# Kernel optimization log

Hardware: AMD Instinct MI355X
Metric: run time of the kernel (lower is better)

## Reference

```python
import jax, jax.numpy as jnp
import numpy as np

B, T, F_, S, H = 4096, 128, 96, 128, 512
IMPUTE_WEIGHT = 0.3
L1, L2 = 0.01, 0.1


def setup_inputs() -> dict:
    key = jax.random.key(0)
    ks = jax.random.split(key, 28)
    def n(k, shape, s=0.05):
        return jax.random.normal(k, shape, jnp.float32) * s
    return dict(
        values=jax.random.normal(ks[0], (B, T, F_), jnp.float32),
        masks=jax.random.bernoulli(ks[1], 0.8, (B, T, F_)).astype(jnp.float32),
        deltas=jax.random.uniform(ks[2], (B, T, F_), jnp.float32, 0.0, 5.0),
        statics=jax.random.normal(ks[3], (B, S), jnp.float32),
        static_masks=jax.random.bernoulli(ks[4], 0.8, (B, S)).astype(jnp.float32),
        labels=jax.random.bernoulli(ks[5], 0.5, (B,)).astype(jnp.float32),
        fr_W=n(ks[6], (S, S)), fr_b=n(ks[7], (S,)),
        d1_W=n(ks[8], (H, S)), d1_b=n(ks[9], (H,)),
        d2_W=n(ks[10], (H, H)), d2_b=n(ks[11], (H,)),
        d3_W=n(ks[12], (H, H)), d3_b=n(ks[13], (H,)),
        td_W=n(ks[14], (H, F_)), td_b=n(ks[15], (H,)),
        hist_W=n(ks[16], (F_, H)), hist_b=n(ks[17], (F_,)),
        st_W=n(ks[18], (F_, S)), st_b=n(ks[19], (F_,)),
        real_W=n(ks[20], (F_, F_)), real_b=n(ks[21], (F_,)),
        lstm_Wih=n(ks[22], (4 * H, 2 * F_)), lstm_Whh=n(ks[23], (4 * H, H)),
        lstm_bih=n(ks[24], (4 * H,)), lstm_bhh=n(ks[25], (4 * H,)),
        out_W=n(ks[26], (1, H)), out_b=n(ks[27], (1,)),
    )


def reference(values, masks, deltas, statics, static_masks, labels,
              fr_W, fr_b, d1_W, d1_b, d2_W, d2_b, d3_W, d3_b,
              td_W, td_b, hist_W, hist_b, st_W, st_b, real_W, real_b,
              lstm_Wih, lstm_Whh, lstm_bih, lstm_bhh, out_W, out_b):
    sg = jax.lax.stop_gradient
    # ---- MultiModal (dropout = identity in inference) ----
    s_h = statics @ fr_W.T + fr_b
    s_c = static_masks * statics + (1.0 - static_masks) * s_h
    s_tc = s_c
    s_loss = jnp.sum(jnp.abs(statics - s_c) * static_masks) / (jnp.sum(static_masks) + 1e-5)
    s_loss = s_loss + IMPUTE_WEIGHT * L2 * jnp.sum(jnp.abs(jnp.diagonal(sg(fr_W))))
    h = jax.nn.relu(s_c @ d1_W.T + d1_b)
    h = jax.nn.relu(h @ d2_W.T + d2_b)
    h = jax.nn.relu(h @ d3_W.T + d3_b)                 # initial hidden state
    c = jnp.zeros((values.shape[0], H), values.dtype)
    st_term = s_tc @ st_W.T + st_b

    def step(carry, xs):
        h, c, xl = carry
        x, m, d = xs                                   # each [B, F_]
        gamma = jnp.exp(-jax.nn.relu(d @ td_W.T + td_b))
        h = h * gamma
        x_c = (x @ real_W.T + real_b) + (h @ hist_W.T + hist_b) + st_term
        xl = xl + jnp.sum(jnp.abs(x - x_c) * m) / (jnp.sum(m) + 1e-5)
        c_c = m * x + (1.0 - m) * x_c
        inp = jnp.concatenate([c_c, m], axis=1)        # [B, 2*F_]
        gates = inp @ lstm_Wih.T + lstm_bih + h @ lstm_Whh.T + lstm_bhh
        i, f, g, o = jnp.split(gates, 4, axis=1)       # torch LSTMCell gate order
        c = jax.nn.sigmoid(f) * c + jax.nn.sigmoid(i) * jnp.tanh(g)
        h = jax.nn.sigmoid(o) * jnp.tanh(c)
        return (h, c, xl), c_c

    xs = (jnp.swapaxes(values, 0, 1), jnp.swapaxes(masks, 0, 1), jnp.swapaxes(deltas, 0, 1))
    (h, c, x_loss), imps = jax.lax.scan(step, (h, c, jnp.float32(0.0)), xs)
    imputations = jnp.swapaxes(imps, 0, 1)             # [B, T, F_]

    y_h = h @ out_W.T + out_b                          # [B, 1]
    z = y_h[:, 0]
    # BCE with logits, mean reduction (stable form)
    y_loss = jnp.mean(jnp.maximum(z, 0.0) - z * labels + jnp.log1p(jnp.exp(-jnp.abs(z))))
    # regularizers on .data (stop-gradient in torch semantics)
    r_loss = L1 * (jnp.sum(jnp.abs(sg(real_W))) + jnp.sum(jnp.abs(sg(hist_W))) + jnp.sum(jnp.abs(sg(st_W))))
    r_loss = r_loss + L2 * jnp.sum(jnp.abs(jnp.diagonal(sg(real_W))))
    loss = y_loss + r_loss + IMPUTE_WEIGHT * x_loss + s_loss
    return (loss, jax.nn.sigmoid(y_h), imputations)
```

## Files before the change

### kernel.cpp

```cpp
#include <hip/hip_runtime.h>
#include <math.h>

#define Bn 4096
#define Tn 128
#define Fn 96
#define Sn 128
#define Hn 512

typedef __attribute__((ext_vector_type(8))) short bf16x8;
typedef __attribute__((ext_vector_type(4))) float f32x4;

#define GC(p) ((const __attribute__((address_space(1))) void*)(p))
#define LC(p) ((__attribute__((address_space(3))) void*)(p))

__device__ __forceinline__ short tobf(float f){
  unsigned u = __float_as_uint(f);
  unsigned r = (u + 0x7fffu + ((u>>16)&1u)) >> 16;
  return (short)r;
}
__device__ __forceinline__ float bf2f(short s){
  return __uint_as_float(((unsigned)(unsigned short)s)<<16);
}
__device__ __forceinline__ float sigmf_(float x){ return 1.0f/(1.0f+expf(-x)); }

__device__ __forceinline__ int haddr(int row, int k){
  int c = k & 63;
  return ((k>>6)<<10) + (row<<6) + ((((c>>3) ^ (row&7)))<<3) + (c&7);
}
__device__ __forceinline__ int haddr128(int row, int k){
  int c = k & 63;
  return ((k>>6)<<13) + (row<<6) + ((((c>>3) ^ (row&7)))<<3) + (c&7);
}

__device__ __forceinline__ void stage_tile(const short* gsrc, size_t sstride, int k0,
                                           short* lt, int rows, int wid, int lane, int nw){
  int calls = rows >> 3;
  for (int c = wid; c < calls; c += nw){
    int r = (c<<3) + (lane>>3);
    int ch = (lane&7) ^ (r&7);
    const short* gp = gsrc + (size_t)r*sstride + k0 + (ch<<3);
    __builtin_amdgcn_global_load_lds(GC(gp), LC(lt + (c<<9)), 16, 0, 0);
  }
}
__device__ __forceinline__ bf16x8 frag(const short* lt, int row, int ch){
  return *(const bf16x8*)(lt + (row<<6) + ((ch ^ (row&7))<<3));
}


__global__ void k_pack_td(const float* __restrict__ tdW, short* __restrict__ tdWp){
  int i = blockIdx.x*256 + threadIdx.x;
  if (i >= 512*128) return;
  int n = i>>7, k = i&127;
  tdWp[i] = (k < Fn) ? tobf(tdW[n*Fn + k]) : (short)0;
}
__global__ void k_pack_x(const float* __restrict__ realW, const float* __restrict__ histW,
                         const float* __restrict__ realb, const float* __restrict__ histb,
                         short* __restrict__ Wxp, float* __restrict__ bxp){
  int i = blockIdx.x*256 + threadIdx.x;
  if (i < Fn) bxp[i] = realb[i] + histb[i];
  if (i >= Fn*640) return;
  int f = i/640, k = i - f*640;
  float v = 0.f;
  if (k < 512) v = histW[f*Hn + k];
  else if (k < 608) v = realW[f*Fn + (k-512)];
  Wxp[i] = tobf(v);
}
__global__ void k_pack_g(const float* __restrict__ Wih, const float* __restrict__ Whh,
                         const float* __restrict__ bih, const float* __restrict__ bhh,
                         short* __restrict__ Wgp, float* __restrict__ bgp){
  int i = blockIdx.x*256 + threadIdx.x;
  if (i >= 16*128*704) return;
  int k = i % 704; int nc = i / 704;
  int pb = nc >> 7, ncol = nc & 127;
  int jj = pb*32 + (ncol >> 2), g = ncol & 3;
  int n = g*Hn + jj;
  float v;
  if (k < 512) v = Whh[(size_t)n*Hn + k];
  else if (k < 608) v = Wih[(size_t)n*192 + (k-512)];
  else v = Wih[(size_t)n*192 + 96 + (k-608)];
  Wgp[i] = tobf(v);
  if (k == 0) bgp[nc] = bih[n] + bhh[n];
}
__global__ void k_cvt(const float* __restrict__ src, short* __restrict__ dst, int n){
  int i = blockIdx.x*256 + threadIdx.x;
  if (i < n) dst[i] = tobf(src[i]);
}


__global__ void k_static(const float* __restrict__ statics, const float* __restrict__ smask,
                         const float* __restrict__ frW, const float* __restrict__ frb,
                         float* __restrict__ s_c){
  __shared__ float row[Sn];
  int b = blockIdx.x, j = threadIdx.x;
  row[j] = statics[b*Sn + j];
  __syncthreads();
  float acc = frb[j];
  #pragma unroll 4
  for (int k = 0; k < Sn; k++) acc += row[k] * frW[j*Sn + k];
  float m = smask[b*Sn + j];
  s_c[b*Sn + j] = m * row[j] + (1.0f - m) * acc;
}

template<int K, bool RELU, bool WF32>
__global__ __launch_bounds__(512) void k_gemm(const short* __restrict__ A,
    const short* __restrict__ B, const float* __restrict__ bias,
    short* __restrict__ outb, float* __restrict__ outf){
  __shared__ __align__(16) short stA[2][8192], stB[2][8192];
  const int tid = threadIdx.x, lane = tid&63, wid = tid>>6;
  const int mb = blockIdx.x >> 2, nb = blockIdx.x & 3;
  const int r0 = mb*128, c0 = nb*128;
  const int wM = wid>>1, wN = wid&1, lr = lane&15, lq = lane>>4;
  f32x4 acc[2][4];
  #pragma unroll
  for (int m=0;m<2;m++)
    #pragma unroll
    for (int n=0;n<4;n++) acc[m][n] = (f32x4){0,0,0,0};
  constexpr int NS = K/64;
  stage_tile(A + (size_t)r0*K, K, 0, stA[0], 128, wid, lane, 8);
  stage_tile(B + (size_t)c0*K, K, 0, stB[0], 128, wid, lane, 8);
  __syncthreads();
  for (int kc=0; kc<NS; kc++){
    if (kc < NS-1){
      stage_tile(A + (size_t)r0*K, K, (kc+1)*64, stA[(kc+1)&1], 128, wid, lane, 8);
      stage_tile(B + (size_t)c0*K, K, (kc+1)*64, stB[(kc+1)&1], 128, wid, lane, 8);
    }
    #pragma unroll
    for (int kk=0;kk<2;kk++){
      int ch = (kk<<2) + lq;
      bf16x8 af[2];
      #pragma unroll
      for (int m=0;m<2;m++) af[m] = frag(stA[kc&1], wM*32 + m*16 + lr, ch);
      #pragma unroll
      for (int n=0;n<4;n++){
        bf16x8 bf = frag(stB[kc&1], wN*64 + n*16 + lr, ch);
        #pragma unroll
        for (int m=0;m<2;m++)
          acc[m][n] = __builtin_amdgcn_mfma_f32_16x16x32_bf16(af[m], bf, acc[m][n],0,0,0);
      }
    }
    __syncthreads();
  }
  #pragma unroll
  for (int m=0;m<2;m++)
    #pragma unroll
    for (int n=0;n<4;n++){
      int col = c0 + wN*64 + n*16 + lr;
      float bv = bias[col];
      #pragma unroll
      for (int reg=0;reg<4;reg++){
        int row = r0 + wM*32 + m*16 + (lq<<2) + reg;
        float v = acc[m][n][reg] + bv;
        if (RELU) v = fmaxf(v, 0.f);
        outb[(size_t)row*512 + col] = tobf(v);
        if (WF32) outf[(size_t)row*512 + col] = v;
      }
    }
}

template<int K, int N, bool RELU>
__global__ void k_mlp(const float* __restrict__ in, const float* __restrict__ W,
                      const float* __restrict__ bias, float* __restrict__ out){
  __shared__ float row[K];
  int b = blockIdx.x;
  for (int i = threadIdx.x; i < K; i += blockDim.x) row[i] = in[b*K + i];
  __syncthreads();
  for (int n = threadIdx.x; n < N; n += blockDim.x){
    float acc = bias[n];
    #pragma unroll 4
    for (int k = 0; k < K; k++) acc += row[k] * W[n*K + k];
    if (RELU) acc = fmaxf(acc, 0.0f);
    out[b*N + n] = acc;
  }
}

__global__ __launch_bounds__(512) void k_dec0(
    const float* __restrict__ deltas, const short* __restrict__ tdWp,
    const float* __restrict__ tdb, const float* __restrict__ h_g,
    short* __restrict__ inp){
  __shared__ __align__(16) short Adel[2*1024];
  __shared__ __align__(16) short Bbig[65536];
  const int tid = threadIdx.x, lane = tid&63, wid = tid>>6;
  const int r0 = blockIdx.x*16;
  const int lr = lane&15, lq = lane>>4;

  float4 dv4;
  const bool act = tid < 384;
  int ar=0, af0=0;
  if (act){
    ar = tid/24; af0 = (tid - ar*24)*4;
    dv4 = *(const float4*)(deltas + (size_t)(r0+ar)*Tn*Fn + af0);
  }
  float hreg[16];
  #pragma unroll
  for (int nq=0;nq<4;nq++){
    int col = nq*128 + wid*16 + lr;
    #pragma unroll
    for (int reg=0;reg<4;reg++)
      hreg[nq*4+reg] = h_g[(size_t)(r0 + (lq<<2) + reg)*Hn + col];
  }
  #pragma unroll
  for (int s=0; s<8; s++)
    stage_tile(tdWp + (size_t)((s>>1)*128)*128, 128, (s&1)*64, Bbig + s*8192, 128, wid, lane, 8);
  if (act){
    #pragma unroll
    for (int j=0;j<4;j++)
      Adel[haddr(ar, af0+j)] = tobf(((const float*)&dv4)[j]);
  }
  { int r = tid>>5, cz = tid&31; Adel[haddr(r, 96+cz)] = 0; }
  __syncthreads();

  f32x4 accd[4];
  #pragma unroll
  for (int q=0;q<4;q++) accd[q] = (f32x4){0,0,0,0};
  #pragma unroll
  for (int s=0; s<8; s++){
    int nq = s>>1, kc = s&1;
    #pragma unroll
    for (int kk=0;kk<2;kk++){
      int ch = (kk<<2) + lq;
      bf16x8 afr = frag(Adel + kc*1024, lr, ch);
      bf16x8 bfr = frag(Bbig + s*8192, wid*16 + lr, ch);
      accd[nq] = __builtin_amdgcn_mfma_f32_16x16x32_bf16(afr, bfr, accd[nq], 0,0,0);
    }
  }
  #pragma unroll
  for (int nq=0;nq<4;nq++){
    int col = nq*128 + wid*16 + lr;
    float tb = tdb[col];
    #pragma unroll
    for (int reg=0;reg<4;reg++){
      int row = (lq<<2) + reg;
      float v = accd[nq][reg] + tb;
      inp[(size_t)(r0+row)*704 + col] = tobf(hreg[nq*4+reg] * __expf(-fmaxf(v,0.f)));
    }
  }
}

__global__ __launch_bounds__(512) void k_xc2(int t,
    const float* __restrict__ values, const float* __restrict__ masks,
    const short* __restrict__ Wxp,  const float* __restrict__ bxp,
    const float* __restrict__ st,
    short* __restrict__ inp, float* __restrict__ out_imp,
    float* __restrict__ num, float* __restrict__ den){
  __shared__ __align__(16) short A2[10*1024];
  __shared__ short sm[16*96];
  __shared__ __align__(16) short Bbig[61440];
  __shared__ float wred[8], wred2[8];
  const int tid = threadIdx.x, lane = tid&63, wid = tid>>6;
  const int r0 = blockIdx.x*16;
  const int lr = lane&15, lq = lane>>4;

  float4 xv4, mv4;
  const bool act = tid < 384;
  int ar=0, af0=0;
  if (act){
    ar = tid/24; af0 = (tid - ar*24)*4;
    size_t gb = ((size_t)(r0+ar)*Tn + t)*Fn + af0;
    xv4 = *(const float4*)(values + gb);
    mv4 = *(const float4*)(masks  + gb);
  }
  float streg[4] = {0.f,0.f,0.f,0.f};
  if (wid < 6){
    int f = wid*16 + lr;
    #pragma unroll
    for (int reg=0;reg<4;reg++)
      streg[reg] = st[(size_t)(r0 + (lq<<2) + reg)*Fn + f];
  }

  for (int c2 = wid; c2 < 16; c2 += 8){
    int chunk = c2 >> 1, rg = c2 & 1;
    int r = rg*8 + (lane>>3);
    int ch = (lane&7) ^ (r&7);
    const short* gp = inp + (size_t)(r0 + r)*704 + chunk*64 + (ch<<3);
    __builtin_amdgcn_global_load_lds(GC(gp), LC(A2 + chunk*1024 + rg*512), 16, 0, 0);
  }
  #pragma unroll
  for (int kx=0; kx<10; kx++)
    stage_tile(Wxp, 640, kx*64, Bbig + kx*6144, 96, wid, lane, 8);

  if (act){
    #pragma unroll
    for (int j=0;j<4;j++){
      int f = af0 + j;
      float xv = ((const float*)&xv4)[j];
      float mv = ((const float*)&mv4)[j];
      sm[ar*96 + f] = tobf(mv);
      inp[(size_t)(r0+ar)*704 + 608 + f] = tobf(mv);
      A2[haddr(ar, 512+f)] = tobf(xv);
    }
  }
  { int r = tid>>5, cz = tid&31; A2[haddr(r, 608+cz)] = 0; }
  __syncthreads();

  f32x4 accx = (f32x4){0,0,0,0};
  if (wid < 6){
    #pragma unroll
    for (int kx=0; kx<10; kx++)
      #pragma unroll
      for (int kk=0;kk<2;kk++){
        int ch = (kk<<2) + lq;
        bf16x8 afr = frag(A2 + kx*1024, lr, ch);
        bf16x8 bfr = frag(Bbig + kx*6144, wid*16 + lr, ch);
        accx = __builtin_amdgcn_mfma_f32_16x16x32_bf16(afr, bfr, accx, 0,0,0);
      }
  }
  float lsum = 0.f, msum = 0.f;
  if (wid < 6){
    int f = wid*16 + lr;
    float bx = bxp[f];
    #pragma unroll
    for (int reg=0;reg<4;reg++){
      int row = (lq<<2) + reg;
      float xcv = accx[reg] + bx + streg[reg];
      float xv = bf2f(A2[haddr(row, 512+f)]);
      float mv = bf2f(sm[row*96 + f]);
      lsum += fabsf(xv - xcv)*mv;
      msum += mv;
      float cc = mv*xv + (1.f-mv)*xcv;
      inp[(size_t)(r0+row)*704 + 512 + f] = tobf(cc);
      out_imp[((size_t)(r0+row)*Tn + t)*Fn + f] = cc;
    }
  }
  #pragma unroll
  for (int o=32;o>0;o>>=1){ lsum += __shfl_down(lsum, o); msum += __shfl_down(msum, o); }
  if (lane==0){ wred[wid] = lsum; wred2[wid] = msum; }
  __syncthreads();
  if (tid==0){
    float s2 = 0.f, s3 = 0.f;
    #pragma unroll
    for (int w2=0;w2<8;w2++){ s2 += wred[w2]; s3 += wred2[w2]; }
    atomicAdd(&num[t], s2);
    atomicAdd(&den[t], s3);
  }
}

__global__ __launch_bounds__(512, 4) void k_gates(int t,
    const short* __restrict__ inpR, short* __restrict__ inpW,
    const short* __restrict__ Wgp, const float* __restrict__ bgp,
    const float* __restrict__ deltas, const short* __restrict__ tdWp,
    const float* __restrict__ tdb,
    float* __restrict__ h_g, float* __restrict__ c_g){
  __shared__ __align__(16) short SMEM[32768];
  const int tid = threadIdx.x, lane = tid&63, wid = tid>>6;
  const int mb = blockIdx.x & 31, pb = blockIdx.x >> 5;
  const int r0 = mb*128;
  const short* gA = inpR + (size_t)r0*704;
  const short* gB = Wgp + (size_t)pb*128*704;
  const int wM = wid>>1, wN = wid&1, lr = lane&15, lq = lane>>4;
  const bool hg = (t+1 < Tn);
  f32x4 acc[2][4];
  #pragma unroll
  for (int m=0;m<2;m++)
    #pragma unroll
    for (int n=0;n<4;n++) acc[m][n] = (f32x4){0,0,0,0};

  stage_tile(gA, 704, 0, SMEM, 128, wid, lane, 8);
  stage_tile(gB, 704, 0, SMEM + 16384, 128, wid, lane, 8);
  __syncthreads();

  for (int kc=0; kc<11; kc++){
    if (kc < 10){
      stage_tile(gA, 704, (kc+1)*64, SMEM + ((kc+1)&1)*8192, 128, wid, lane, 8);
      stage_tile(gB, 704, (kc+1)*64, SMEM + 16384 + ((kc+1)&1)*8192, 128, wid, lane, 8);
    }
    #pragma unroll
    for (int kk=0;kk<2;kk++){
      int ch = (kk<<2) + lq;
      bf16x8 af[2];
      #pragma unroll
      for (int m=0;m<2;m++) af[m] = frag(SMEM + (kc&1)*8192, wM*32 + m*16 + lr, ch);
      #pragma unroll
      for (int n=0;n<4;n++){
        bf16x8 bf = frag(SMEM + 16384 + (kc&1)*8192, wN*64 + n*16 + lr, ch);
        #pragma unroll
        for (int m=0;m<2;m++)
          acc[m][n] = __builtin_amdgcn_mfma_f32_16x16x32_bf16(af[m], bf, acc[m][n],0,0,0);
      }
    }
    __syncthreads();
  }

  float dreg[24];
  const int drow = tid>>2, dc0 = (tid&3)*24;
  if (hg){
    size_t gb = ((size_t)(r0+drow)*Tn + (t+1))*Fn + dc0;
    #pragma unroll
    for (int q=0;q<6;q++){
      float4 v4 = *(const float4*)(deltas + gb + q*4);
      dreg[q*4+0]=v4.x; dreg[q*4+1]=v4.y; dreg[q*4+2]=v4.z; dreg[q*4+3]=v4.w;
    }
    stage_tile(tdWp + (size_t)(pb*32)*128, 128, 0,  SMEM + 16384, 32, wid, lane, 8);
    stage_tile(tdWp + (size_t)(pb*32)*128, 128, 64, SMEM + 18432, 32, wid, lane, 8);
  }

  const int g = lane&3;
  const float s_  = (g==2) ? 2.0f : -1.0f;
  const float ca_ = (g==2) ? -2.0f : 1.0f;
  const float cb_ = (g==2) ? 1.0f : 0.0f;
  float hnew[2][4];
  #pragma unroll
  for (int m=0;m<2;m++){
    int row = r0 + wM*32 + m*16 + (lq<<2) + g;
    #pragma unroll
    for (int n=0;n<4;n++){
      int colbase = wN*64 + n*16 + lr;
      float b = bgp[pb*128 + colbase];
      float q0 = 1.f/(1.f+__expf(s_*(acc[m][n][0]+b))); float a0 = q0*ca_+cb_;
      float q1 = 1.f/(1.f+__expf(s_*(acc[m][n][1]+b))); float a1 = q1*ca_+cb_;
      float q2 = 1.f/(1.f+__expf(s_*(acc[m][n][2]+b))); float a2 = q2*ca_+cb_;
      float q3 = 1.f/(1.f+__expf(s_*(acc[m][n][3]+b))); float a3 = q3*ca_+cb_;
      int i1=g^1, i2=g^2, i3=g^3;
      float p1 = (i1==0)?a0:(i1==1)?a1:(i1==2)?a2:a3;
      float p2 = (i2==0)?a0:(i2==1)?a1:(i2==2)?a2:a3;
      float p3 = (i3==0)?a0:(i3==1)?a1:(i3==2)?a2:a3;
      float ow = (g==0)?a0:(g==1)?a1:(g==2)?a2:a3;
      float t1 = __shfl_xor(p1, 1, 64);
      float t2 = __shfl_xor(p2, 2, 64);
      float t3 = __shfl_xor(p3, 3, 64);
      float si = (g==0)?ow:(g==1)?t1:(g==2)?t2:t3;
      float sf = (g==1)?ow:(g==0)?t1:(g==3)?t2:t3;
      float tg = (g==2)?ow:(g==3)?t1:(g==0)?t2:t3;
      float so = (g==3)?ow:(g==2)?t1:(g==1)?t2:t3;
      int jh = pb*32 + (colbase>>2);
      size_t idx = (size_t)row*Hn + jh;
      float co = c_g[idx];
      float cn = sf*co + si*tg;
      float targ = fminf(fmaxf(2.0f*cn,-60.f),60.f);
      float e = __expf(targ); float th = (e-1.f)/(e+1.f);
      c_g[idx] = cn;
      float hv = so*th;
      h_g[idx] = hv;
      hnew[m][n] = hv;
    }
  }

  if (hg){
    #pragma unroll
    for (int j=0;j<24;j++){
      int cdx = dc0 + j;
      SMEM[haddr128(drow, cdx)] = tobf(dreg[j]);
    }
    #pragma unroll
    for (int j=0;j<8;j++){
      int cdx = 96 + (tid&3)*8 + j;
      SMEM[haddr128(drow, cdx)] = 0;
    }
    __syncthreads();

    f32x4 gv[2];
    gv[0]=(f32x4){0,0,0,0}; gv[1]=(f32x4){0,0,0,0};
    #pragma unroll
    for (int kc=0;kc<2;kc++)
      #pragma unroll
      for (int kk=0;kk<2;kk++){
        int ch = (kk<<2) + lq;
        bf16x8 afr = frag(SMEM + kc*8192, wid*16 + lr, ch);
        #pragma unroll
        for (int n=0;n<2;n++)
          gv[n] = __builtin_amdgcn_mfma_f32_16x16x32_bf16(afr,
                    frag(SMEM + 16384 + kc*2048, n*16 + lr, ch), gv[n], 0,0,0);
      }
    float* vlds = (float*)(SMEM + 20480);
    #pragma unroll
    for (int n=0;n<2;n++)
      #pragma unroll
      for (int reg=0;reg<4;reg++)
        vlds[(wid*16 + (lq<<2) + reg)*33 + n*16 + lr] = gv[n][reg];
    __syncthreads();

    #pragma unroll
    for (int m=0;m<2;m++){
      int rowl = wM*32 + m*16 + (lq<<2) + g;
      #pragma unroll
      for (int n=0;n<4;n++){
        int jl = (wN*64 + n*16 + lr)>>2;
        float v = vlds[rowl*33 + jl] + tdb[pb*32 + jl];
        float gam = __expf(-fmaxf(v, 0.f));
        inpW[(size_t)(r0+rowl)*704 + pb*32 + jl] = tobf(hnew[m][n] * gam);
      }
    }
  }
}


__global__ void k_out(const float* __restrict__ h_g, const float* __restrict__ outW,
                      const float* __restrict__ outb, const float* __restrict__ labels,
                      float* __restrict__ out_sig, float* __restrict__ yacc){
  int b = blockIdx.x, lane = threadIdx.x;
  float s = 0.f;
  for (int k = lane; k < Hn; k += 64) s += h_g[(size_t)b*Hn + k] * outW[k];
  #pragma unroll
  for (int o = 32; o > 0; o >>= 1) s += __shfl_down(s, o);
  if (lane == 0){
    float z = s + outb[0];
    out_sig[b] = sigmf_(z);
    float yl = fmaxf(z, 0.f) - z*labels[b] + log1pf(expf(-fabsf(z)));
    atomicAdd(yacc, yl);
  }
}

__global__ void k_loss(const float* __restrict__ realW, const float* __restrict__ histW,
                       const float* __restrict__ stW,   const float* __restrict__ frW,
                       const float* __restrict__ num,   const float* __restrict__ den,
                       const float* __restrict__ yacc,  float* __restrict__ out0){
  int tid = threadIdx.x;
  float r1 = 0.f;
  for (int i = tid; i < Fn*Fn; i += 256) r1 += fabsf(realW[i]);
  for (int i = tid; i < Fn*Hn; i += 256) r1 += fabsf(histW[i]);
  for (int i = tid; i < Fn*Sn; i += 256) r1 += fabsf(stW[i]);
  float rd = 0.f;
  for (int i = tid; i < Fn; i += 256) rd += fabsf(realW[i*Fn + i]);
  float fd = 0.f;
  for (int i = tid; i < Sn; i += 256) fd += fabsf(frW[i*Sn + i]);
  float xl = 0.f;
  for (int t = tid; t < Tn; t += 256) xl += num[t] / (den[t] + 1e-5f);
  float v = 0.01f*r1 + 0.1f*rd + 0.3f*xl + 0.03f*fd;
  __shared__ float red[256];
  red[tid] = v; __syncthreads();
  for (int o = 128; o > 0; o >>= 1){ if (tid < o) red[tid] += red[tid + o]; __syncthreads(); }
  if (tid == 0) out0[0] = red[0] + yacc[0] / (float)Bn;
}


extern "C" void kernel_launch(void* const* d_in, const int* in_sizes, int n_in,
                              void* d_out, int out_size, void* d_ws, size_t ws_size,
                              hipStream_t stream){
  const float* values = (const float*)d_in[0];
  const float* masks  = (const float*)d_in[1];
  const float* deltas = (const float*)d_in[2];
  const float* statics= (const float*)d_in[3];
  const float* smask  = (const float*)d_in[4];
  const float* labels = (const float*)d_in[5];
  const float* frW = (const float*)d_in[6];
  const float* frb = (const float*)d_in[7];
  const float* d1W = (const float*)d_in[8];
  const float* d1b = (const float*)d_in[9];
  const float* d2W = (const float*)d_in[10];
  const float* d2b = (const float*)d_in[11];
  const float* d3W = (const float*)d_in[12];
  const float* d3b = (const float*)d_in[13];
  const float* tdW = (const float*)d_in[14];
  const float* tdb = (const float*)d_in[15];
  const float* histW = (const float*)d_in[16];
  const float* histb = (const float*)d_in[17];
  const float* stW = (const float*)d_in[18];
  const float* stb = (const float*)d_in[19];
  const float* realW = (const float*)d_in[20];
  const float* realb = (const float*)d_in[21];
  const float* Wih = (const float*)d_in[22];
  const float* Whh = (const float*)d_in[23];
  const float* bih = (const float*)d_in[24];
  const float* bhh = (const float*)d_in[25];
  const float* outW = (const float*)d_in[26];
  const float* outb = (const float*)d_in[27];

  float* out0    = (float*)d_out;
  float* out_sig = out0 + 1;
  float* out_imp = out0 + 1 + Bn;

  float* wsf  = (float*)d_ws;
  float* s_c  = wsf;  wsf += Bn*Sn;
  float* h    = wsf;  wsf += (size_t)Bn*Hn;
  float* c    = wsf;  wsf += (size_t)Bn*Hn;
  float* st   = wsf;  wsf += Bn*Fn;
  float* den  = wsf;  wsf += Tn;
  float* num  = wsf;  wsf += Tn;
  float* yacc = num + Tn;
  wsf += 1;
  float* bxp  = wsf;  wsf += 128;
  float* bgp  = wsf;  wsf += 2048;
  size_t off = ((size_t)(wsf - (float*)d_ws) + 3u) & ~(size_t)3u;
  short* wss  = (short*)((float*)d_ws + off);
  short* tdWp = wss;  wss += 512*128;
  short* Wxp  = wss;  wss += 96*640;
  short* Wgp  = wss;  wss += (size_t)16*128*704;
  short* inp0 = wss;  wss += (size_t)Bn*704;
  short* inp1 = wss;  wss += (size_t)Bn*704;
  short* wd1  = wss;  wss += 512*128;
  short* wd2  = wss;  wss += 512*512;
  short* wd3  = wss;  wss += 512*512;
  short* act0 = wss;  wss += (size_t)Bn*128;
  short* actA = wss;  wss += (size_t)Bn*512;
  short* actB = wss;  wss += (size_t)Bn*512;

  hipMemsetAsync(c,   0, (size_t)Bn*Hn*sizeof(float), stream);
  hipMemsetAsync(den, 0, (2*Tn + 1)*sizeof(float), stream);

  k_pack_td<<<(512*128+255)/256, 256, 0, stream>>>(tdW, tdWp);
  k_pack_x <<<(96*640+255)/256, 256, 0, stream>>>(realW, histW, realb, histb, Wxp, bxp);
  k_pack_g <<<(16*128*704+255)/256, 256, 0, stream>>>(Wih, Whh, bih, bhh, Wgp, bgp);
  k_cvt<<<(512*128+255)/256, 256, 0, stream>>>(d1W, wd1, 512*128);
  k_cvt<<<(512*512+255)/256, 256, 0, stream>>>(d2W, wd2, 512*512);
  k_cvt<<<(512*512+255)/256, 256, 0, stream>>>(d3W, wd3, 512*512);

  k_static<<<Bn, Sn, 0, stream>>>(statics, smask, frW, frb, s_c);
  k_cvt<<<(Bn*Sn+255)/256, 256, 0, stream>>>(s_c, act0, Bn*Sn);
  k_gemm<128, true,  false><<<128, 512, 0, stream>>>(act0, wd1, d1b, actA, (float*)nullptr);
  k_gemm<512, true,  false><<<128, 512, 0, stream>>>(actA, wd2, d2b, actB, (float*)nullptr);
  k_gemm<512, true,  true ><<<128, 512, 0, stream>>>(actB, wd3, d3b, actA, h);
  k_mlp<Sn, Fn, false><<<Bn, 256, 0, stream>>>(s_c, stW, stb, st);

  k_dec0<<<Bn/16, 512, 0, stream>>>(deltas, tdWp, tdb, h, inp0);

  for (int t = 0; t < Tn; t++){
    short* iR = (t & 1) ? inp1 : inp0;
    short* iW = (t & 1) ? inp0 : inp1;
    k_xc2  <<<Bn/16,       512, 0, stream>>>(t, values, masks, Wxp, bxp, st,
                                             iR, out_imp, num, den);
    k_gates<<<(Bn/128)*16, 512, 0, stream>>>(t, iR, iW, Wgp, bgp,
                                             deltas, tdWp, tdb, h, c);
  }

  k_out<<<Bn, 64, 0, stream>>>(h, outW, outb, labels, out_sig, yacc);
  k_loss<<<1, 256, 0, stream>>>(realW, histW, stW, frW, num, den, yacc, out0);
}
```

Baseline: 5.327 ms.

## Fuse per-step imputation and LSTM gate kernels into one block-local kernel

```diff
diff --git a/kernel.cpp b/kernel.cpp
--- a/kernel.cpp
+++ b/kernel.cpp
@@ -23,13 +23,12 @@
 }
 __device__ __forceinline__ float sigmf_(float x){ return 1.0f/(1.0f+expf(-x)); }
 
+__device__ __forceinline__ int sw64(int row, int c){
+  return (row<<6) + ((((c>>3) ^ (row&7)))<<3) + (c&7);
+}
 __device__ __forceinline__ int haddr(int row, int k){
   int c = k & 63;
   return ((k>>6)<<10) + (row<<6) + ((((c>>3) ^ (row&7)))<<3) + (c&7);
-}
-__device__ __forceinline__ int haddr128(int row, int k){
-  int c = k & 63;
-  return ((k>>6)<<13) + (row<<6) + ((((c>>3) ^ (row&7)))<<3) + (c&7);
 }
 
 __device__ __forceinline__ void stage_tile(const short* gsrc, size_t sstride, int k0,
@@ -69,10 +68,10 @@
                          const float* __restrict__ bih, const float* __restrict__ bhh,
                          short* __restrict__ Wgp, float* __restrict__ bgp){
   int i = blockIdx.x*256 + threadIdx.x;
-  if (i >= 16*128*704) return;
+  if (i >= 2048*704) return;
   int k = i % 704; int nc = i / 704;
-  int pb = nc >> 7, ncol = nc & 127;
-  int jj = pb*32 + (ncol >> 2), g = ncol & 3;
+  int pb = nc >> 8, ncol = nc & 255;
+  int jj = pb*64 + (ncol >> 2), g = ncol & 3;
   int n = g*Hn + jj;
   float v;
   if (k < 512) v = Whh[(size_t)n*Hn + k];
@@ -231,149 +230,151 @@
     for (int reg=0;reg<4;reg++){
       int row = (lq<<2) + reg;
       float v = accd[nq][reg] + tb;
-      inp[(size_t)(r0+row)*704 + col] = tobf(hreg[nq*4+reg] * __expf(-fmaxf(v,0.f)));
-    }
-  }
-}
-
-__global__ __launch_bounds__(512) void k_xc2(int t,
+      inp[(size_t)(r0+row)*512 + col] = tobf(hreg[nq*4+reg] * __expf(-fmaxf(v,0.f)));
+    }
+  }
+}
+
+__global__ __launch_bounds__(512) void k_sg(int t,
     const float* __restrict__ values, const float* __restrict__ masks,
+    const float* __restrict__ deltas,
     const short* __restrict__ Wxp,  const float* __restrict__ bxp,
-    const float* __restrict__ st,
-    short* __restrict__ inp, float* __restrict__ out_imp,
-    float* __restrict__ num, float* __restrict__ den){
-  __shared__ __align__(16) short A2[10*1024];
-  __shared__ short sm[16*96];
-  __shared__ __align__(16) short Bbig[61440];
+    const float* __restrict__ st,   const short* __restrict__ Wgp,
+    const float* __restrict__ bgp,  const short* __restrict__ tdWp,
+    const float* __restrict__ tdb,
+    const short* __restrict__ inpR, short* __restrict__ inpW,
+    float* __restrict__ h_g, float* __restrict__ c_g,
+    float* __restrict__ out_imp, float* __restrict__ num, float* __restrict__ den){
+  __shared__ __align__(16) short P[73728];
   __shared__ float wred[8], wred2[8];
-  const int tid = threadIdx.x, lane = tid&63, wid = tid>>6;
-  const int r0 = blockIdx.x*16;
+  short* ccm  = P;
+  short* xA   = P + 24576;
+  short* aD   = P + 40960;
+  short* bD   = P + 57344;
+  short* gB   = P + 40960;
+  short* tdS  = P + 40960;
+  float* vlds = (float*)(P + 49152);
+  const int tid = threadIdx.x, lane = tid&63, w = tid>>6;
+  const int pb = blockIdx.x & 7, mb = blockIdx.x >> 3;
+  const int r0 = mb*128;
   const int lr = lane&15, lq = lane>>4;
-
-  float4 xv4, mv4;
-  const bool act = tid < 384;
-  int ar=0, af0=0;
-  if (act){
-    ar = tid/24; af0 = (tid - ar*24)*4;
-    size_t gb = ((size_t)(r0+ar)*Tn + t)*Fn + af0;
-    xv4 = *(const float4*)(values + gb);
-    mv4 = *(const float4*)(masks  + gb);
-  }
-  float streg[4] = {0.f,0.f,0.f,0.f};
-  if (wid < 6){
-    int f = wid*16 + lr;
-    #pragma unroll
-    for (int reg=0;reg<4;reg++)
-      streg[reg] = st[(size_t)(r0 + (lq<<2) + reg)*Fn + f];
-  }
-
-  for (int c2 = wid; c2 < 16; c2 += 8){
-    int chunk = c2 >> 1, rg = c2 & 1;
-    int r = rg*8 + (lane>>3);
-    int ch = (lane&7) ^ (r&7);
-    const short* gp = inp + (size_t)(r0 + r)*704 + chunk*64 + (ch<<3);
-    __builtin_amdgcn_global_load_lds(GC(gp), LC(A2 + chunk*1024 + rg*512), 16, 0, 0);
-  }
-  #pragma unroll
-  for (int kx=0; kx<10; kx++)
-    stage_tile(Wxp, 640, kx*64, Bbig + kx*6144, 96, wid, lane, 8);
-
-  if (act){
-    #pragma unroll
-    for (int j=0;j<4;j++){
-      int f = af0 + j;
-      float xv = ((const float*)&xv4)[j];
-      float mv = ((const float*)&mv4)[j];
-      sm[ar*96 + f] = tobf(mv);
-      inp[(size_t)(r0+ar)*704 + 608 + f] = tobf(mv);
-      A2[haddr(ar, 512+f)] = tobf(xv);
-    }
-  }
-  { int r = tid>>5, cz = tid&31; A2[haddr(r, 608+cz)] = 0; }
+  const bool hg = (t+1 < Tn);
+
+  const int ir = tid>>2, ic0 = (tid&3)*24;
+  float xr[24], mr[24];
+  {
+    size_t gb2 = ((size_t)(r0+ir)*Tn + t)*Fn + ic0;
+    #pragma unroll
+    for (int q=0;q<6;q++){
+      float4 xv = *(const float4*)(values + gb2 + q*4);
+      float4 mv = *(const float4*)(masks  + gb2 + q*4);
+      xr[q*4+0]=xv.x; xr[q*4+1]=xv.y; xr[q*4+2]=xv.z; xr[q*4+3]=xv.w;
+      mr[q*4+0]=mv.x; mr[q*4+1]=mv.y; mr[q*4+2]=mv.z; mr[q*4+3]=mv.w;
+    }
+  }
+  stage_tile(inpR + (size_t)r0*512, 512, 0, aD, 128, w, lane, 8);
+  stage_tile(Wxp, 640, 0, bD, 96, w, lane, 8);
+
+  #pragma unroll
+  for (int j=0;j<24;j++){
+    int f = ic0 + j;
+    xA[((f>>6)<<13) + sw64(ir, f&63)] = tobf(xr[j]);
+    int km = 608 + f;
+    ccm[(((km>>6)-8)<<13) + sw64(ir, km&63)] = tobf(mr[j]);
+  }
+  #pragma unroll
+  for (int j=0;j<8;j++){
+    int cz = 32 + (tid&3)*8 + j;
+    xA[8192 + sw64(ir, cz)] = 0;
+  }
   __syncthreads();
 
-  f32x4 accx = (f32x4){0,0,0,0};
-  if (wid < 6){
-    #pragma unroll
-    for (int kx=0; kx<10; kx++)
+  f32x4 accx[8];
+  #pragma unroll
+  for (int m=0;m<8;m++) accx[m] = (f32x4){0,0,0,0};
+  for (int kx=0; kx<10; kx++){
+    if (kx < 9){
+      if (kx+1 < 8)
+        stage_tile(inpR + (size_t)r0*512, 512, (kx+1)*64, aD + ((kx+1)&1)*8192, 128, w, lane, 8);
+      stage_tile(Wxp, 640, (kx+1)*64, bD + ((kx+1)&1)*6144, 96, w, lane, 8);
+    }
+    const short* Ac = (kx<8) ? (aD + (kx&1)*8192) : (xA + (kx-8)*8192);
+    const short* Bc = bD + (kx&1)*6144;
+    if (w < 6){
       #pragma unroll
       for (int kk=0;kk<2;kk++){
         int ch = (kk<<2) + lq;
-        bf16x8 afr = frag(A2 + kx*1024, lr, ch);
-        bf16x8 bfr = frag(Bbig + kx*6144, wid*16 + lr, ch);
-        accx = __builtin_amdgcn_mfma_f32_16x16x32_bf16(afr, bfr, accx, 0,0,0);
+        bf16x8 bfr = frag(Bc, w*16 + lr, ch);
+        #pragma unroll
+        for (int m=0;m<8;m++)
+          accx[m] = __builtin_amdgcn_mfma_f32_16x16x32_bf16(frag(Ac, m*16+lr, ch), bfr, accx[m],0,0,0);
       }
+    }
+    __syncthreads();
   }
   float lsum = 0.f, msum = 0.f;
-  if (wid < 6){
-    int f = wid*16 + lr;
+  if (w < 6){
+    int f = w*16 + lr;
     float bx = bxp[f];
     #pragma unroll
-    for (int reg=0;reg<4;reg++){
-      int row = (lq<<2) + reg;
-      float xcv = accx[reg] + bx + streg[reg];
-      float xv = bf2f(A2[haddr(row, 512+f)]);
-      float mv = bf2f(sm[row*96 + f]);
-      lsum += fabsf(xv - xcv)*mv;
-      msum += mv;
-      float cc = mv*xv + (1.f-mv)*xcv;
-      inp[(size_t)(r0+row)*704 + 512 + f] = tobf(cc);
-      out_imp[((size_t)(r0+row)*Tn + t)*Fn + f] = cc;
-    }
+    for (int m=0;m<8;m++)
+      #pragma unroll
+      for (int reg=0;reg<4;reg++){
+        int row = m*16 + (lq<<2) + reg;
+        float xcv = accx[m][reg] + bx + st[(size_t)(r0+row)*Fn + f];
+        float xv = bf2f(xA[((f>>6)<<13) + sw64(row, f&63)]);
+        int km = 608 + f;
+        float mv = bf2f(ccm[(((km>>6)-8)<<13) + sw64(row, km&63)]);
+        lsum += fabsf(xv - xcv)*mv;
+        msum += mv;
+        float cc = mv*xv + (1.f-mv)*xcv;
+        ccm[((f>>6)<<13) + sw64(row, f&63)] = tobf(cc);
+        if (pb == 0) out_imp[((size_t)(r0+row)*Tn + t)*Fn + f] = cc;
+      }
   }
   #pragma unroll
   for (int o=32;o>0;o>>=1){ lsum += __shfl_down(lsum, o); msum += __shfl_down(msum, o); }
-  if (lane==0){ wred[wid] = lsum; wred2[wid] = msum; }
+  if (lane==0){ wred[w] = lsum; wred2[w] = msum; }
   __syncthreads();
-  if (tid==0){
+  if (tid==0 && pb==0){
     float s2 = 0.f, s3 = 0.f;
     #pragma unroll
     for (int w2=0;w2<8;w2++){ s2 += wred[w2]; s3 += wred2[w2]; }
     atomicAdd(&num[t], s2);
     atomicAdd(&den[t], s3);
   }
-}
-
-__global__ __launch_bounds__(512, 4) void k_gates(int t,
-    const short* __restrict__ inpR, short* __restrict__ inpW,
-    const short* __restrict__ Wgp, const float* __restrict__ bgp,
-    const float* __restrict__ deltas, const short* __restrict__ tdWp,
-    const float* __restrict__ tdb,
-    float* __restrict__ h_g, float* __restrict__ c_g){
-  __shared__ __align__(16) short SMEM[32768];
-  const int tid = threadIdx.x, lane = tid&63, wid = tid>>6;
-  const int mb = blockIdx.x & 31, pb = blockIdx.x >> 5;
-  const int r0 = mb*128;
-  const short* gA = inpR + (size_t)r0*704;
-  const short* gB = Wgp + (size_t)pb*128*704;
-  const int wM = wid>>1, wN = wid&1, lr = lane&15, lq = lane>>4;
-  const bool hg = (t+1 < Tn);
-  f32x4 acc[2][4];
-  #pragma unroll
-  for (int m=0;m<2;m++)
+
+  const short* WgB = Wgp + (size_t)pb*256*704;
+  stage_tile(inpR + (size_t)r0*512, 512, 0, xA, 128, w, lane, 8);
+  stage_tile(WgB, 704, 0, gB, 256, w, lane, 8);
+  __syncthreads();
+
+  const int wM = w>>2, wN = w&3;
+  f32x4 acc[4][4];
+  #pragma unroll
+  for (int m=0;m<4;m++)
     #pragma unroll
     for (int n=0;n<4;n++) acc[m][n] = (f32x4){0,0,0,0};
-
-  stage_tile(gA, 704, 0, SMEM, 128, wid, lane, 8);
-  stage_tile(gB, 704, 0, SMEM + 16384, 128, wid, lane, 8);
-  __syncthreads();
 
   for (int kc=0; kc<11; kc++){
     if (kc < 10){
-      stage_tile(gA, 704, (kc+1)*64, SMEM + ((kc+1)&1)*8192, 128, wid, lane, 8);
-      stage_tile(gB, 704, (kc+1)*64, SMEM + 16384 + ((kc+1)&1)*8192, 128, wid, lane, 8);
-    }
+      if (kc+1 < 8)
+        stage_tile(inpR + (size_t)r0*512, 512, (kc+1)*64, xA + ((kc+1)&1)*8192, 128, w, lane, 8);
+      stage_tile(WgB, 704, (kc+1)*64, gB + ((kc+1)&1)*16384, 256, w, lane, 8);
+    }
+    const short* Ac = (kc<8) ? (xA + (kc&1)*8192) : (ccm + (kc-8)*8192);
+    const short* Bc = gB + (kc&1)*16384;
     #pragma unroll
     for (int kk=0;kk<2;kk++){
       int ch = (kk<<2) + lq;
-      bf16x8 af[2];
-      #pragma unroll
-      for (int m=0;m<2;m++) af[m] = frag(SMEM + (kc&1)*8192, wM*32 + m*16 + lr, ch);
+      bf16x8 af[4];
+      #pragma unroll
+      for (int m=0;m<4;m++) af[m] = frag(Ac, wM*64 + m*16 + lr, ch);
       #pragma unroll
       for (int n=0;n<4;n++){
-        bf16x8 bf = frag(SMEM + 16384 + (kc&1)*8192, wN*64 + n*16 + lr, ch);
+        bf16x8 bf = frag(Bc, wN*64 + n*16 + lr, ch);
         #pragma unroll
-        for (int m=0;m<2;m++)
+        for (int m=0;m<4;m++)
           acc[m][n] = __builtin_amdgcn_mfma_f32_16x16x32_bf16(af[m], bf, acc[m][n],0,0,0);
       }
     }
@@ -381,30 +382,29 @@
   }
 
   float dreg[24];
-  const int drow = tid>>2, dc0 = (tid&3)*24;
   if (hg){
-    size_t gb = ((size_t)(r0+drow)*Tn + (t+1))*Fn + dc0;
+    size_t gb2 = ((size_t)(r0+ir)*Tn + (t+1))*Fn + ic0;
     #pragma unroll
     for (int q=0;q<6;q++){
-      float4 v4 = *(const float4*)(deltas + gb + q*4);
+      float4 v4 = *(const float4*)(deltas + gb2 + q*4);
       dreg[q*4+0]=v4.x; dreg[q*4+1]=v4.y; dreg[q*4+2]=v4.z; dreg[q*4+3]=v4.w;
     }
-    stage_tile(tdWp + (size_t)(pb*32)*128, 128, 0,  SMEM + 16384, 32, wid, lane, 8);
-    stage_tile(tdWp + (size_t)(pb*32)*128, 128, 64, SMEM + 18432, 32, wid, lane, 8);
+    stage_tile(tdWp + (size_t)(pb*64)*128, 128, 0,  tdS,        64, w, lane, 8);
+    stage_tile(tdWp + (size_t)(pb*64)*128, 128, 64, tdS + 4096, 64, w, lane, 8);
   }
 
   const int g = lane&3;
   const float s_  = (g==2) ? 2.0f : -1.0f;
   const float ca_ = (g==2) ? -2.0f : 1.0f;
   const float cb_ = (g==2) ? 1.0f : 0.0f;
-  float hnew[2][4];
-  #pragma unroll
-  for (int m=0;m<2;m++){
-    int row = r0 + wM*32 + m*16 + (lq<<2) + g;
+  float hnew[4][4];
+  #pragma unroll
+  for (int m=0;m<4;m++){
+    int row = r0 + wM*64 + m*16 + (lq<<2) + g;
     #pragma unroll
     for (int n=0;n<4;n++){
       int colbase = wN*64 + n*16 + lr;
-      float b = bgp[pb*128 + colbase];
+      float b = bgp[pb*256 + colbase];
       float q0 = 1.f/(1.f+__expf(s_*(acc[m][n][0]+b))); float a0 = q0*ca_+cb_;
       float q1 = 1.f/(1.f+__expf(s_*(acc[m][n][1]+b))); float a1 = q1*ca_+cb_;
       float q2 = 1.f/(1.f+__expf(s_*(acc[m][n][2]+b))); float a2 = q2*ca_+cb_;
@@ -421,7 +421,7 @@
       float sf = (g==1)?ow:(g==0)?t1:(g==3)?t2:t3;
       float tg = (g==2)?ow:(g==3)?t1:(g==0)?t2:t3;
       float so = (g==3)?ow:(g==2)?t1:(g==1)?t2:t3;
-      int jh = pb*32 + (colbase>>2);
+      int jh = pb*64 + (colbase>>2);
       size_t idx = (size_t)row*Hn + jh;
       float co = c_g[idx];
       float cn = sf*co + si*tg;
@@ -437,46 +437,46 @@
   if (hg){
     #pragma unroll
     for (int j=0;j<24;j++){
-      int cdx = dc0 + j;
-      SMEM[haddr128(drow, cdx)] = tobf(dreg[j]);
+      int cdx = ic0 + j;
+      xA[((cdx>>6)<<13) + sw64(ir, cdx&63)] = tobf(dreg[j]);
     }
     #pragma unroll
     for (int j=0;j<8;j++){
-      int cdx = 96 + (tid&3)*8 + j;
-      SMEM[haddr128(drow, cdx)] = 0;
+      int cz = 32 + (tid&3)*8 + j;
+      xA[8192 + sw64(ir, cz)] = 0;
     }
     __syncthreads();
 
-    f32x4 gv[2];
-    gv[0]=(f32x4){0,0,0,0}; gv[1]=(f32x4){0,0,0,0};
+    f32x4 gv[4];
+    #pragma unroll
+    for (int n=0;n<4;n++) gv[n] = (f32x4){0,0,0,0};
     #pragma unroll
     for (int kc=0;kc<2;kc++)
       #pragma unroll
       for (int kk=0;kk<2;kk++){
         int ch = (kk<<2) + lq;
-        bf16x8 afr = frag(SMEM + kc*8192, wid*16 + lr, ch);
+        bf16x8 afr = frag(xA + kc*8192, w*16 + lr, ch);
         #pragma unroll
-        for (int n=0;n<2;n++)
+        for (int n=0;n<4;n++)
           gv[n] = __builtin_amdgcn_mfma_f32_16x16x32_bf16(afr,
-                    frag(SMEM + 16384 + kc*2048, n*16 + lr, ch), gv[n], 0,0,0);
+                    frag(tdS + kc*4096, n*16 + lr, ch), gv[n], 0,0,0);
       }
-    float* vlds = (float*)(SMEM + 20480);
-    #pragma unroll
-    for (int n=0;n<2;n++)
+    #pragma unroll
+    for (int n=0;n<4;n++)
       #pragma unroll
       for (int reg=0;reg<4;reg++)
-        vlds[(wid*16 + (lq<<2) + reg)*33 + n*16 + lr] = gv[n][reg];
+        vlds[(w*16 + (lq<<2) + reg)*65 + n*16 + lr] = gv[n][reg];
     __syncthreads();
 
     #pragma unroll
-    for (int m=0;m<2;m++){
-      int rowl = wM*32 + m*16 + (lq<<2) + g;
+    for (int m=0;m<4;m++){
+      int rowl = wM*64 + m*16 + (lq<<2) + g;
       #pragma unroll
       for (int n=0;n<4;n++){
         int jl = (wN*64 + n*16 + lr)>>2;
-        float v = vlds[rowl*33 + jl] + tdb[pb*32 + jl];
+        float v = vlds[rowl*65 + jl] + tdb[pb*64 + jl];
         float gam = __expf(-fmaxf(v, 0.f));
-        inpW[(size_t)(r0+rowl)*704 + pb*32 + jl] = tobf(hnew[m][n] * gam);
+        inpW[(size_t)(r0+rowl)*512 + pb*64 + jl] = tobf(hnew[m][n] * gam);
       }
     }
   }
@@ -573,9 +573,9 @@
   short* wss  = (short*)((float*)d_ws + off);
   short* tdWp = wss;  wss += 512*128;
   short* Wxp  = wss;  wss += 96*640;
-  short* Wgp  = wss;  wss += (size_t)16*128*704;
-  short* inp0 = wss;  wss += (size_t)Bn*704;
-  short* inp1 = wss;  wss += (size_t)Bn*704;
+  short* Wgp  = wss;  wss += (size_t)2048*704;
+  short* inp0 = wss;  wss += (size_t)Bn*512;
+  short* inp1 = wss;  wss += (size_t)Bn*512;
   short* wd1  = wss;  wss += 512*128;
   short* wd2  = wss;  wss += 512*512;
   short* wd3  = wss;  wss += 512*512;
@@ -588,7 +588,7 @@
 
   k_pack_td<<<(512*128+255)/256, 256, 0, stream>>>(tdW, tdWp);
   k_pack_x <<<(96*640+255)/256, 256, 0, stream>>>(realW, histW, realb, histb, Wxp, bxp);
-  k_pack_g <<<(16*128*704+255)/256, 256, 0, stream>>>(Wih, Whh, bih, bhh, Wgp, bgp);
+  k_pack_g <<<(2048*704+255)/256, 256, 0, stream>>>(Wih, Whh, bih, bhh, Wgp, bgp);
   k_cvt<<<(512*128+255)/256, 256, 0, stream>>>(d1W, wd1, 512*128);
   k_cvt<<<(512*512+255)/256, 256, 0, stream>>>(d2W, wd2, 512*512);
   k_cvt<<<(512*512+255)/256, 256, 0, stream>>>(d3W, wd3, 512*512);
@@ -605,10 +605,9 @@
   for (int t = 0; t < Tn; t++){
     short* iR = (t & 1) ? inp1 : inp0;
     short* iW = (t & 1) ? inp0 : inp1;
-    k_xc2  <<<Bn/16,       512, 0, stream>>>(t, values, masks, Wxp, bxp, st,
-                                             iR, out_imp, num, den);
-    k_gates<<<(Bn/128)*16, 512, 0, stream>>>(t, iR, iW, Wgp, bgp,
-                                             deltas, tdWp, tdb, h, c);
+    k_sg<<<256, 512, 0, stream>>>(t, values, masks, deltas, Wxp, bxp, st,
+                                  Wgp, bgp, tdWp, tdb, iR, iW, h, c,
+                                  out_imp, num, den);
   }
 
   k_out<<<Bn, 64, 0, stream>>>(h, outW, outb, labels, out_sig, yacc);
```

Measured after the change: 8.052 ms. 51.1% more time.
